# Kernel tuning notes

Measured on AMD Instinct MI355X. Metric: run time of the kernel, lower is better.

Reference implementation:

```python
import jax, jax.numpy as jnp
import numpy as np

NUM_GRAPHS = 2048


def gcn_conv(x, W, b, edge, N):
    # PyG GCNConv: x' = D^{-1/2} (A + I) D^{-1/2} (x W) + b
    src, dst = edge[0], edge[1]
    loop = jnp.arange(N, dtype=src.dtype)
    src = jnp.concatenate([src, loop])
    dst = jnp.concatenate([dst, loop])
    h = x @ W  # [N, out]
    deg = jax.ops.segment_sum(jnp.ones(dst.shape, x.dtype), dst, num_segments=N)
    dinv = jnp.where(deg > 0, jax.lax.rsqrt(deg), 0.0)
    norm = dinv[src] * dinv[dst]  # [E+N]
    out = jax.ops.segment_sum(h[src] * norm[:, None], dst, num_segments=N)
    return out + b


def pool_max_mean(x, batch, G):
    mx = jax.ops.segment_max(x, batch, num_segments=G)
    mx = jnp.where(jnp.isfinite(mx), mx, 0.0)  # guard empty segments
    s = jax.ops.segment_sum(x, batch, num_segments=G)
    cnt = jax.ops.segment_sum(jnp.ones((x.shape[0],), x.dtype), batch, num_segments=G)
    mean = s / jnp.maximum(cnt, 1.0)[:, None]
    return mx, mean


def setup_inputs() -> dict:
    key = jax.random.key(0)
    ks = jax.random.split(key, 20)
    F, CE, SE, DD = 64, 64, 32, 128
    Nc, Ec, Ns, Es = 100000, 1250000, 100000, 1250000

    def glorot(k, shape):
        fan_in, fan_out = shape[0], shape[1]
        lim = np.sqrt(6.0 / (fan_in + fan_out)).astype(np.float32)
        return jax.random.uniform(k, shape, jnp.float32, -lim, lim)

    inp = {
        "c": jax.random.normal(ks[0], (Nc, F), jnp.float32),
        "c_edge": jax.random.randint(ks[1], (2, Ec), 0, Nc),
        "c_batch": jnp.sort(jax.random.randint(ks[2], (Nc,), 0, NUM_GRAPHS)),
        "s": jax.random.normal(ks[3], (Ns, F), jnp.float32),
        "s_edge": jax.random.randint(ks[4], (2, Es), 0, Ns),
        "s_batch": jnp.sort(jax.random.randint(ks[5], (Ns,), 0, NUM_GRAPHS)),
        "Wc0": glorot(ks[6], (F, CE)), "bc0": jnp.zeros((CE,), jnp.float32),
        "Wc1": glorot(ks[7], (CE, CE)), "bc1": jnp.zeros((CE,), jnp.float32),
        "Wc2": glorot(ks[8], (CE, CE)), "bc2": jnp.zeros((CE,), jnp.float32),
        "Ws0": glorot(ks[9], (F, SE)), "bs0": jnp.zeros((SE,), jnp.float32),
        "Ws1": glorot(ks[10], (SE, SE)), "bs1": jnp.zeros((SE,), jnp.float32),
        "Ws2": glorot(ks[11], (SE, SE)), "bs2": jnp.zeros((SE,), jnp.float32),
        "Wd": glorot(ks[12], ((CE + SE) * 2, DD)), "bd": jnp.zeros((DD,), jnp.float32),
        "Wo": glorot(ks[13], (DD, 1)), "bo": jnp.zeros((1,), jnp.float32),
    }
    return inp


def reference(c, c_edge, c_batch, s, s_edge, s_batch,
              Wc0, bc0, Wc1, bc1, Wc2, bc2,
              Ws0, bs0, Ws1, bs1, Ws2, bs2,
              Wd, bd, Wo, bo):
    Nc, Ns = c.shape[0], s.shape[0]
    cro = jax.nn.relu(gcn_conv(c, Wc0, bc0, c_edge, Nc))
    cro = jax.nn.relu(gcn_conv(cro, Wc1, bc1, c_edge, Nc))
    cro = jax.nn.relu(gcn_conv(cro, Wc2, bc2, c_edge, Nc))
    solv = jax.nn.relu(gcn_conv(s, Ws0, bs0, s_edge, Ns))
    solv = jax.nn.relu(gcn_conv(solv, Ws1, bs1, s_edge, Ns))
    solv = jax.nn.relu(gcn_conv(solv, Ws2, bs2, s_edge, Ns))
    c_mx, c_mean = pool_max_mean(cro, c_batch, NUM_GRAPHS)
    s_mx, s_mean = pool_max_mean(solv, s_batch, NUM_GRAPHS)
    embed = jnp.concatenate([c_mx, c_mean, s_mx, s_mean], axis=1)  # [G, 192]
    dense = jax.nn.relu(embed @ Wd + bd)
    out = dense @ Wo + bo  # [G, 1]
    return out, embed
```

## Files before the change

kernel.cpp:

```cpp
#include <hip/hip_runtime.h>
#include <hip/hip_fp16.h>
#include <math.h>


static inline int cdiv(int a, int b) { return (a + b - 1) / b; }

#define BUCKET_CAP 8192
#define P1_CHUNK   4096

__global__ void zero_int(int* __restrict__ p, int n) {
    int i = blockIdx.x * blockDim.x + threadIdx.x;
    if (i < n) p[i] = 0;
}

__global__ __launch_bounds__(256) void p1_partition(const int* __restrict__ c_edge, int Ec,
                                                    const int* __restrict__ s_edge, int Es,
                                                    int Nc_pad, int Etot, int nbuck,
                                                    int* __restrict__ bucket_fill,
                                                    unsigned* __restrict__ pk) {
    __shared__ unsigned       wbuf[P1_CHUNK];
    __shared__ unsigned short bbuf[P1_CHUNK];
    __shared__ int            hist[512];
    int e0 = blockIdx.x * P1_CHUNK;
    int n  = Etot - e0;
    if (n > P1_CHUNK) n = P1_CHUNK;
    for (int i = threadIdx.x; i < nbuck; i += 256) hist[i] = 0;
    __syncthreads();
    for (int i = threadIdx.x; i < n; i += 256) {
        int e = e0 + i, src, g;
        if (e < Ec) { src = c_edge[e]; g = c_edge[Ec + e]; }
        else        { int e2 = e - Ec; src = s_edge[e2]; g = Nc_pad + s_edge[Es + e2]; }
        int b   = g >> 9;
        wbuf[i] = ((unsigned)(g & 511) << 17) | (unsigned)src;
        bbuf[i] = (unsigned short)b;
        atomicAdd(&hist[b], 1);
    }
    __syncthreads();
    for (int i = threadIdx.x; i < nbuck; i += 256) {
        int h = hist[i];
        hist[i] = h ? atomicAdd(&bucket_fill[i], h) : 0;
    }
    __syncthreads();
    for (int i = threadIdx.x; i < n; i += 256) {
        int b    = bbuf[i];
        int slot = atomicAdd(&hist[b], 1);
        if (slot < BUCKET_CAP) pk[(size_t)b * BUCKET_CAP + slot] = wbuf[i];
    }
}

__global__ __launch_bounds__(512) void p2_scanbuckets(const int* __restrict__ fill, int nbuck,
                                                      int* __restrict__ basearr,
                                                      int* __restrict__ off_all, int Ntot_pad, int Etot) {
    __shared__ int sh[512];
    int v = (threadIdx.x < nbuck) ? fill[threadIdx.x] : 0;
    sh[threadIdx.x] = v;
    __syncthreads();
    for (int ofs = 1; ofs < 512; ofs <<= 1) {
        int t = (threadIdx.x >= ofs) ? sh[threadIdx.x - ofs] : 0;
        __syncthreads();
        sh[threadIdx.x] += t;
        __syncthreads();
    }
    if (threadIdx.x < nbuck) basearr[threadIdx.x] = sh[threadIdx.x] - v;
    if (threadIdx.x == 0) off_all[Ntot_pad] = Etot;
}

__global__ __launch_bounds__(512) void p3_build(const unsigned* __restrict__ pk,
                                                const int* __restrict__ fillarr,
                                                const int* __restrict__ basearr,
                                                int* __restrict__ off_all,
                                                float* __restrict__ dinv,
                                                int* __restrict__ csr) {
    __shared__ int sh[512];
    int b    = blockIdx.x;
    int fill = fillarr[b];
    if (fill > BUCKET_CAP) fill = BUCKET_CAP;
    int base = basearr[b];
    const unsigned* reg = pk + (size_t)b * BUCKET_CAP;
    sh[threadIdx.x] = 0;
    __syncthreads();
    for (int i = threadIdx.x; i < fill; i += 512) atomicAdd(&sh[reg[i] >> 17], 1);
    __syncthreads();
    int cnt = sh[threadIdx.x];
    for (int ofs = 1; ofs < 512; ofs <<= 1) {
        int t = (threadIdx.x >= ofs) ? sh[threadIdx.x - ofs] : 0;
        __syncthreads();
        sh[threadIdx.x] += t;
        __syncthreads();
    }
    int excl = sh[threadIdx.x] - cnt;
    int node = b * 512 + threadIdx.x;
    off_all[node] = base + excl;
    dinv[node]    = rsqrtf((float)(cnt + 1));
    __syncthreads();
    sh[threadIdx.x] = excl;
    __syncthreads();
    for (int i = threadIdx.x; i < fill; i += 512) {
        unsigned w    = reg[i];
        int      slot = atomicAdd(&sh[w >> 17], 1);
        csr[base + slot] = (int)(w & 0x1FFFFu);
    }
}

template <int K, int M, typename TIN>
__device__ void gemm_body(int bid, const TIN* __restrict__ X, const float* __restrict__ W,
                          const float* __restrict__ dinv, __half* __restrict__ H, int N,
                          char* smem_) {
    constexpr int CG = M / 4, RG = 256 / CG, RB = RG * 4, RBP = RB + 4;
    float* Xs = (float*)smem_;
    float* Ws = Xs + K * RBP;
    const int t    = threadIdx.x;
    const int row0 = bid * RB;

    for (int idx = t; idx < K * M; idx += 256) Ws[idx] = W[idx];

    if constexpr (sizeof(TIN) == 4) {
        constexpr int NF4 = RB * K / 4;
        for (int idx = t; idx < NF4; idx += 256) {
            int row = idx / (K / 4), k4 = idx % (K / 4);
            float4 v = make_float4(0.f, 0.f, 0.f, 0.f);
            int gr = row0 + row;
            if (gr < N) v = *(const float4*)((const float*)X + (size_t)gr * K + k4 * 4);
            Xs[(k4 * 4 + 0) * RBP + row] = v.x;
            Xs[(k4 * 4 + 1) * RBP + row] = v.y;
            Xs[(k4 * 4 + 2) * RBP + row] = v.z;
            Xs[(k4 * 4 + 3) * RBP + row] = v.w;
        }
    } else {
        constexpr int NF8 = RB * K / 8;
        for (int idx = t; idx < NF8; idx += 256) {
            int row = idx / (K / 8), k8 = idx % (K / 8);
            int gr = row0 + row;
            union { float4 f4; __half2 h2[4]; } u;
            u.f4 = make_float4(0.f, 0.f, 0.f, 0.f);
            if (gr < N) u.f4 = *(const float4*)((const __half*)X + (size_t)gr * K + k8 * 8);
#pragma unroll
            for (int q = 0; q < 4; ++q) {
                float2 pq = __half22float2(u.h2[q]);
                Xs[(k8 * 8 + 2 * q + 0) * RBP + row] = pq.x;
                Xs[(k8 * 8 + 2 * q + 1) * RBP + row] = pq.y;
            }
        }
    }
    __syncthreads();

    const int cc = t % CG, rr = t / CG;
    float acc[4][4] = {};
#pragma unroll 4
    for (int k = 0; k < K; k++) {
        float4 xv = *(const float4*)(Xs + k * RBP + rr * 4);
        float4 wv = *(const float4*)(Ws + k * M + cc * 4);
        acc[0][0] += xv.x * wv.x; acc[0][1] += xv.x * wv.y; acc[0][2] += xv.x * wv.z; acc[0][3] += xv.x * wv.w;
        acc[1][0] += xv.y * wv.x; acc[1][1] += xv.y * wv.y; acc[1][2] += xv.y * wv.z; acc[1][3] += xv.y * wv.w;
        acc[2][0] += xv.z * wv.x; acc[2][1] += xv.z * wv.y; acc[2][2] += xv.z * wv.z; acc[2][3] += xv.z * wv.w;
        acc[3][0] += xv.w * wv.x; acc[3][1] += xv.w * wv.y; acc[3][2] += xv.w * wv.z; acc[3][3] += xv.w * wv.w;
    }

#pragma unroll
    for (int i = 0; i < 4; i++) {
        int gr = row0 + rr * 4 + i;
        if (gr < N) {
            float sc = dinv[gr];
            __half2* dp = (__half2*)(H + (size_t)gr * M + cc * 4);
            dp[0] = __floats2half2_rn(acc[i][0] * sc, acc[i][1] * sc);
            dp[1] = __floats2half2_rn(acc[i][2] * sc, acc[i][3] * sc);
        }
    }
}

__device__ __forceinline__ float4 load4h(const float2* __restrict__ base, size_t idx) {
    float2 r = base[idx];
    union { float2 f2; __half2 h2[2]; } u;
    u.f2 = r;
    float2 a = __half22float2(u.h2[0]);
    float2 b = __half22float2(u.h2[1]);
    return make_float4(a.x, a.y, b.x, b.y);
}

template <int M>
__device__ void agg_body(int bid, const __half* __restrict__ H,
                         const int* __restrict__ off_g,
                         const int* __restrict__ csr,
                         const float* __restrict__ dinv_g,
                         const float* __restrict__ b,
                         __half* __restrict__ out, int Nloc) {
    constexpr int L   = M / 4;
    constexpr int NPW = 64 / L;
    int lane = threadIdx.x & 63;
    int wave = threadIdx.x >> 6;
    int fq   = lane & (L - 1);
    int sub  = lane / L;
    int node = (bid * 4 + wave) * NPW + sub;
    if (node >= Nloc) return;
    const float2* H4 = (const float2*)H;
    int j0 = off_g[node], j1 = off_g[node + 1];
    float4 acc = load4h(H4, (size_t)node * L + fq);
    int j = j0;
    for (; j + 8 <= j1; j += 8) {
        int s0 = csr[j],     s1 = csr[j + 1], s2 = csr[j + 2], s3 = csr[j + 3];
        int s4 = csr[j + 4], s5 = csr[j + 5], s6 = csr[j + 6], s7 = csr[j + 7];
        float4 a0 = load4h(H4, (size_t)s0 * L + fq);
        float4 a1 = load4h(H4, (size_t)s1 * L + fq);
        float4 a2 = load4h(H4, (size_t)s2 * L + fq);
        float4 a3 = load4h(H4, (size_t)s3 * L + fq);
        float4 a4 = load4h(H4, (size_t)s4 * L + fq);
        float4 a5 = load4h(H4, (size_t)s5 * L + fq);
        float4 a6 = load4h(H4, (size_t)s6 * L + fq);
        float4 a7 = load4h(H4, (size_t)s7 * L + fq);
        acc.x += (a0.x + a1.x + a2.x + a3.x) + (a4.x + a5.x + a6.x + a7.x);
        acc.y += (a0.y + a1.y + a2.y + a3.y) + (a4.y + a5.y + a6.y + a7.y);
        acc.z += (a0.z + a1.z + a2.z + a3.z) + (a4.z + a5.z + a6.z + a7.z);
        acc.w += (a0.w + a1.w + a2.w + a3.w) + (a4.w + a5.w + a6.w + a7.w);
    }
    for (; j + 4 <= j1; j += 4) {
        int s0 = csr[j], s1 = csr[j + 1], s2 = csr[j + 2], s3 = csr[j + 3];
        float4 a0 = load4h(H4, (size_t)s0 * L + fq);
        float4 a1 = load4h(H4, (size_t)s1 * L + fq);
        float4 a2 = load4h(H4, (size_t)s2 * L + fq);
        float4 a3 = load4h(H4, (size_t)s3 * L + fq);
        acc.x += a0.x + a1.x + a2.x + a3.x;
        acc.y += a0.y + a1.y + a2.y + a3.y;
        acc.z += a0.z + a1.z + a2.z + a3.z;
        acc.w += a0.w + a1.w + a2.w + a3.w;
    }
    for (; j < j1; ++j) {
        float4 a = load4h(H4, (size_t)csr[j] * L + fq);
        acc.x += a.x; acc.y += a.y; acc.z += a.z; acc.w += a.w;
    }
    float  dv = dinv_g[node];
    float4 bb = ((const float4*)b)[fq];
    float  vx = dv * acc.x + bb.x;
    float  vy = dv * acc.y + bb.y;
    float  vz = dv * acc.z + bb.z;
    float  vw = dv * acc.w + bb.w;
    union { float2 f2; __half2 h2[2]; } o;
    o.h2[0] = __floats2half2_rn(vx > 0.f ? vx : 0.f, vy > 0.f ? vy : 0.f);
    o.h2[1] = __floats2half2_rn(vz > 0.f ? vz : 0.f, vw > 0.f ? vw : 0.f);
    ((float2*)out)[(size_t)node * L + fq] = o.f2;
}

__global__ __launch_bounds__(256) void gemmBoth0(const float* __restrict__ Xc, const float* __restrict__ Wc,
                                                 __half* __restrict__ cH, int Nc,
                                                 const float* __restrict__ Xs, const float* __restrict__ Ws,
                                                 __half* __restrict__ sH, int Ns,
                                                 const float* __restrict__ dinv_all, int Nc_pad, int nbC) {
    __shared__ __align__(16) char smem[41984];
    if (blockIdx.x < nbC) gemm_body<64, 64, float>(blockIdx.x, Xc, Wc, dinv_all, cH, Nc, smem);
    else                  gemm_body<64, 32, float>(blockIdx.x - nbC, Xs, Ws, dinv_all + Nc_pad, sH, Ns, smem);
}

__global__ __launch_bounds__(256) void gemmBoth(const __half* __restrict__ Xc, const float* __restrict__ Wc,
                                                __half* __restrict__ cH, int Nc,
                                                const __half* __restrict__ Xs, const float* __restrict__ Ws,
                                                __half* __restrict__ sH, int Ns,
                                                const float* __restrict__ dinv_all, int Nc_pad, int nbC) {
    __shared__ __align__(16) char smem[34816];
    if (blockIdx.x < nbC) gemm_body<64, 64, __half>(blockIdx.x, Xc, Wc, dinv_all, cH, Nc, smem);
    else                  gemm_body<32, 32, __half>(blockIdx.x - nbC, Xs, Ws, dinv_all + Nc_pad, sH, Ns, smem);
}

__global__ __launch_bounds__(256) void aggBoth(const __half* __restrict__ cH, const __half* __restrict__ sH,
                                               const int* __restrict__ off_all, const int* __restrict__ csr_all,
                                               const float* __restrict__ dinv_all,
                                               const float* __restrict__ bc, const float* __restrict__ bs,
                                               __half* __restrict__ outc, __half* __restrict__ outs,
                                               int Nc, int Ns, int Nc_pad, int nbC) {
    if (blockIdx.x < nbC)
        agg_body<64>(blockIdx.x, cH, off_all, csr_all, dinv_all, bc, outc, Nc);
    else
        agg_body<32>(blockIdx.x - nbC, sH, off_all + Nc_pad, csr_all,
                     dinv_all + Nc_pad, bs, outs, Ns);
}

__device__ __forceinline__ int lbound(const int* __restrict__ a, int n, int key) {
    int lo = 0, hi = n;
    while (lo < hi) {
        int mid = (lo + hi) >> 1;
        if (a[mid] < key) lo = mid + 1; else hi = mid;
    }
    return lo;
}

__global__ __launch_bounds__(128) void poolDense(const __half* __restrict__ cX, const int* __restrict__ c_batch, int Nc,
                                                 const __half* __restrict__ sX, const int* __restrict__ s_batch, int Ns,
                                                 const float* __restrict__ Wd, const float* __restrict__ bd,
                                                 const float* __restrict__ Wo, const float* __restrict__ bo,
                                                 float* __restrict__ outv, float* __restrict__ embed) {
    __shared__ float e[192];
    __shared__ float red[128];
    int g = blockIdx.x, t = threadIdx.x;
    if (t < 64) {
        int lo = lbound(c_batch, Nc, g), hi = lbound(c_batch, Nc, g + 1);
        float mx = 0.f, sm = 0.f;
        for (int i = lo; i < hi; ++i) {
            float v = __half2float(cX[(size_t)i * 64 + t]);
            mx = fmaxf(mx, v); sm += v;
        }
        int cn = hi - lo;
        e[t]      = mx;
        e[64 + t] = sm / (float)(cn > 0 ? cn : 1);
    } else if (t < 96) {
        int f  = t - 64;
        int lo = lbound(s_batch, Ns, g), hi = lbound(s_batch, Ns, g + 1);
        float mx = 0.f, sm = 0.f;
        for (int i = lo; i < hi; ++i) {
            float v = __half2float(sX[(size_t)i * 32 + f]);
            mx = fmaxf(mx, v); sm += v;
        }
        int cn = hi - lo;
        e[128 + f] = mx;
        e[160 + f] = sm / (float)(cn > 0 ? cn : 1);
    }
    __syncthreads();
    for (int k = t; k < 192; k += 128) embed[(size_t)g * 192 + k] = e[k];
    float acc = bd[t];
    for (int k = 0; k < 192; ++k) acc += e[k] * Wd[k * 128 + t];
    float d = acc > 0.f ? acc : 0.f;
    red[t]  = d * Wo[t];
    __syncthreads();
    for (int ofs = 64; ofs > 0; ofs >>= 1) {
        if (t < ofs) red[t] += red[t + ofs];
        __syncthreads();
    }
    if (t == 0) outv[g] = red[0] + bo[0];
}


extern "C" void kernel_launch(void* const* d_in, const int* in_sizes, int n_in,
                              void* d_out, int out_size, void* d_ws, size_t ws_size,
                              hipStream_t stream) {
    const float* c       = (const float*)d_in[0];
    const int*   c_edge  = (const int*)d_in[1];
    const int*   c_batch = (const int*)d_in[2];
    const float* s       = (const float*)d_in[3];
    const int*   s_edge  = (const int*)d_in[4];
    const int*   s_batch = (const int*)d_in[5];
    const float* Wc0 = (const float*)d_in[6],  *bc0 = (const float*)d_in[7];
    const float* Wc1 = (const float*)d_in[8],  *bc1 = (const float*)d_in[9];
    const float* Wc2 = (const float*)d_in[10], *bc2 = (const float*)d_in[11];
    const float* Ws0 = (const float*)d_in[12], *bs0 = (const float*)d_in[13];
    const float* Ws1 = (const float*)d_in[14], *bs1 = (const float*)d_in[15];
    const float* Ws2 = (const float*)d_in[16], *bs2 = (const float*)d_in[17];
    const float* Wd  = (const float*)d_in[18], *bd  = (const float*)d_in[19];
    const float* Wo  = (const float*)d_in[20], *bo  = (const float*)d_in[21];

    const int Nc = in_sizes[0] / 64;
    const int Ec = in_sizes[1] / 2;
    const int Ns = in_sizes[3] / 64;
    const int Es = in_sizes[4] / 2;
    const int G  = out_size / 193;
    const int Nc_pad   = cdiv(Nc, 512) * 512;
    const int Ns_pad   = cdiv(Ns, 512) * 512;
    const int Ntot_pad = Nc_pad + Ns_pad;
    const int Etot     = Ec + Es;
    const int nbuck    = Ntot_pad >> 9;

    char* p = (char*)d_ws;
    auto  alloc = [&](size_t bytes) -> void* {
        void* r = (void*)p;
        p += (bytes + 255) & ~(size_t)255;
        return r;
    };
    int*      bucket_fill = (int*)alloc(512 * 4);
    int*      bucket_base = (int*)alloc(512 * 4);
    unsigned* pk          = (unsigned*)alloc((size_t)nbuck * BUCKET_CAP * 4);
    int*      off_all     = (int*)alloc(((size_t)Ntot_pad + 1) * 4);
    int*      csr_all     = (int*)alloc((size_t)Etot * 4);
    float*    dinv_all    = (float*)alloc((size_t)Ntot_pad * 4);
    __half*   bufC        = (__half*)alloc((size_t)Nc * 64 * 2);
    __half*   bufS        = (__half*)alloc((size_t)Ns * 32 * 2);
    __half*   cH          = (__half*)alloc((size_t)Nc * 64 * 2);
    __half*   sH          = (__half*)alloc((size_t)Ns * 32 * 2);

    float* outv  = (float*)d_out;
    float* embed = outv + G;

    const int nbGmC = cdiv(Nc, 64), nbGm0S = cdiv(Ns, 128), nbGmS = cdiv(Ns, 128);
    const int nbAgC = Nc_pad / 16,  nbAgS  = Ns_pad / 32;

    zero_int<<<cdiv(nbuck, 256), 256, 0, stream>>>(bucket_fill, nbuck);
    p1_partition<<<cdiv(Etot, P1_CHUNK), 256, 0, stream>>>(c_edge, Ec, s_edge, Es,
                                                           Nc_pad, Etot, nbuck, bucket_fill, pk);
    p2_scanbuckets<<<1, 512, 0, stream>>>(bucket_fill, nbuck, bucket_base, off_all, Ntot_pad, Etot);
    p3_build<<<nbuck, 512, 0, stream>>>(pk, bucket_fill, bucket_base,
                                        off_all, dinv_all, csr_all);

    gemmBoth0<<<nbGmC + nbGm0S, 256, 0, stream>>>(c, Wc0, cH, Nc, s, Ws0, sH, Ns,
                                                  dinv_all, Nc_pad, nbGmC);
    aggBoth<<<nbAgC + nbAgS, 256, 0, stream>>>(cH, sH, off_all, csr_all, dinv_all,
                                               bc0, bs0, bufC, bufS, Nc, Ns, Nc_pad, nbAgC);
    gemmBoth<<<nbGmC + nbGmS, 256, 0, stream>>>(bufC, Wc1, cH, Nc, bufS, Ws1, sH, Ns,
                                                dinv_all, Nc_pad, nbGmC);
    aggBoth<<<nbAgC + nbAgS, 256, 0, stream>>>(cH, sH, off_all, csr_all, dinv_all,
                                               bc1, bs1, bufC, bufS, Nc, Ns, Nc_pad, nbAgC);
    gemmBoth<<<nbGmC + nbGmS, 256, 0, stream>>>(bufC, Wc2, cH, Nc, bufS, Ws2, sH, Ns,
                                                dinv_all, Nc_pad, nbGmC);
    aggBoth<<<nbAgC + nbAgS, 256, 0, stream>>>(cH, sH, off_all, csr_all, dinv_all,
                                               bc2, bs2, bufC, bufS, Nc, Ns, Nc_pad, nbAgC);

    poolDense<<<G, 128, 0, stream>>>(bufC, c_batch, Nc, bufS, s_batch, Ns,
                                     Wd, bd, Wo, bo, outv, embed);
}
```

Baseline: 418.2 us.

## Replace scalar FP32 GEMM with MFMA f16 matrix-core GEMM for GCN transforms

Rewrites the per-layer dense transform (X·W scaled by dinv) to use the 16x16x32 f16 MFMA instruction. X tiles are staged in LDS as half precision and W is pre-swizzled into the MFMA B-operand layout, replacing the 4x4 register-blocked FP32 FMA loop. This cuts ALU time and LDS footprint. In exchange, the first layer's FP32 inputs and the weights are rounded to fp16, and the output is written as scattered single-half stores, which coalesce less well.

Result: faster. 367.6 us (-12.1%).

```diff
diff --git a/kernel.cpp b/kernel.cpp
--- a/kernel.cpp
+++ b/kernel.cpp
@@ -7,6 +7,9 @@
 
 #define BUCKET_CAP 8192
 #define P1_CHUNK   4096
+
+typedef _Float16 v8h __attribute__((ext_vector_type(8)));
+typedef float    v4f __attribute__((ext_vector_type(4)));
 
 __global__ void zero_int(int* __restrict__ p, int n) {
     int i = blockIdx.x * blockDim.x + threadIdx.x;
@@ -103,67 +106,79 @@
 }
 
 template <int K, int M, typename TIN>
-__device__ void gemm_body(int bid, const TIN* __restrict__ X, const float* __restrict__ W,
+__device__ void gemm_mfma(int bid, const TIN* __restrict__ X, const float* __restrict__ W,
                           const float* __restrict__ dinv, __half* __restrict__ H, int N,
                           char* smem_) {
-    constexpr int CG = M / 4, RG = 256 / CG, RB = RG * 4, RBP = RB + 4;
-    float* Xs = (float*)smem_;
-    float* Ws = Xs + K * RBP;
+    constexpr int RB = 64;
+    constexpr int KP = K + 8;
+    constexpr int NT = M / 16;
+    constexpr int KS = K / 32;
+    _Float16* Xh = (_Float16*)smem_;
+    _Float16* Wz = Xh + RB * KP;
     const int t    = threadIdx.x;
     const int row0 = bid * RB;
 
-    for (int idx = t; idx < K * M; idx += 256) Ws[idx] = W[idx];
-
+    constexpr int WENT = NT * KS * 64;
+    for (int idx = t; idx < WENT; idx += 256) {
+        int lane = idx & 63, rest = idx >> 6;
+        int ks = rest % KS, ntl = rest / KS;
+        int kbase = ks * 32 + (lane >> 4) * 8;
+        int col   = ntl * 16 + (lane & 15);
+        union { float4 f4; _Float16 h[8]; } u;
+#pragma unroll
+        for (int j = 0; j < 8; ++j) u.h[j] = (_Float16)W[(kbase + j) * M + col];
+        *(float4*)(Wz + idx * 8) = u.f4;
+    }
     if constexpr (sizeof(TIN) == 4) {
-        constexpr int NF4 = RB * K / 4;
-        for (int idx = t; idx < NF4; idx += 256) {
+        constexpr int NI = RB * K / 4;
+        for (int idx = t; idx < NI; idx += 256) {
             int row = idx / (K / 4), k4 = idx % (K / 4);
+            int gr = row0 + row;
             float4 v = make_float4(0.f, 0.f, 0.f, 0.f);
-            int gr = row0 + row;
             if (gr < N) v = *(const float4*)((const float*)X + (size_t)gr * K + k4 * 4);
-            Xs[(k4 * 4 + 0) * RBP + row] = v.x;
-            Xs[(k4 * 4 + 1) * RBP + row] = v.y;
-            Xs[(k4 * 4 + 2) * RBP + row] = v.z;
-            Xs[(k4 * 4 + 3) * RBP + row] = v.w;
+            union { float2 f2; _Float16 h[4]; } u;
+            u.h[0] = (_Float16)v.x; u.h[1] = (_Float16)v.y;
+            u.h[2] = (_Float16)v.z; u.h[3] = (_Float16)v.w;
+            *(float2*)(Xh + row * KP + k4 * 4) = u.f2;
         }
     } else {
-        constexpr int NF8 = RB * K / 8;
-        for (int idx = t; idx < NF8; idx += 256) {
+        constexpr int NI = RB * K / 8;
+        for (int idx = t; idx < NI; idx += 256) {
             int row = idx / (K / 8), k8 = idx % (K / 8);
             int gr = row0 + row;
-            union { float4 f4; __half2 h2[4]; } u;
-            u.f4 = make_float4(0.f, 0.f, 0.f, 0.f);
-            if (gr < N) u.f4 = *(const float4*)((const __half*)X + (size_t)gr * K + k8 * 8);
-#pragma unroll
-            for (int q = 0; q < 4; ++q) {
-                float2 pq = __half22float2(u.h2[q]);
-                Xs[(k8 * 8 + 2 * q + 0) * RBP + row] = pq.x;
-                Xs[(k8 * 8 + 2 * q + 1) * RBP + row] = pq.y;
-            }
-        }
-    }
-    __syncthreads();
-
-    const int cc = t % CG, rr = t / CG;
-    float acc[4][4] = {};
-#pragma unroll 4
-    for (int k = 0; k < K; k++) {
-        float4 xv = *(const float4*)(Xs + k * RBP + rr * 4);
-        float4 wv = *(const float4*)(Ws + k * M + cc * 4);
-        acc[0][0] += xv.x * wv.x; acc[0][1] += xv.x * wv.y; acc[0][2] += xv.x * wv.z; acc[0][3] += xv.x * wv.w;
-        acc[1][0] += xv.y * wv.x; acc[1][1] += xv.y * wv.y; acc[1][2] += xv.y * wv.z; acc[1][3] += xv.y * wv.w;
-        acc[2][0] += xv.z * wv.x; acc[2][1] += xv.z * wv.y; acc[2][2] += xv.z * wv.z; acc[2][3] += xv.z * wv.w;
-        acc[3][0] += xv.w * wv.x; acc[3][1] += xv.w * wv.y; acc[3][2] += xv.w * wv.z; acc[3][3] += xv.w * wv.w;
-    }
-
-#pragma unroll
-    for (int i = 0; i < 4; i++) {
-        int gr = row0 + rr * 4 + i;
+            float4 v = make_float4(0.f, 0.f, 0.f, 0.f);
+            if (gr < N) v = *(const float4*)((const __half*)X + (size_t)gr * K + k8 * 8);
+            *(float4*)(Xh + row * KP + k8 * 8) = v;
+        }
+    }
+    __syncthreads();
+
+    const int wave = t >> 6, lane = t & 63;
+    const int quad = lane >> 4, nl = lane & 15;
+    const int rowA = wave * 16 + nl;
+
+    v4f acc[NT];
+#pragma unroll
+    for (int i = 0; i < NT; ++i) acc[i] = (v4f){0.f, 0.f, 0.f, 0.f};
+
+#pragma unroll
+    for (int ks = 0; ks < KS; ++ks) {
+        v8h a = *(const v8h*)(Xh + rowA * KP + ks * 32 + quad * 8);
+#pragma unroll
+        for (int ntl = 0; ntl < NT; ++ntl) {
+            v8h b = *(const v8h*)(Wz + ((ntl * KS + ks) * 64 + lane) * 8);
+            acc[ntl] = __builtin_amdgcn_mfma_f32_16x16x32_f16(a, b, acc[ntl], 0, 0, 0);
+        }
+    }
+
+#pragma unroll
+    for (int r = 0; r < 4; ++r) {
+        int gr = row0 + wave * 16 + quad * 4 + r;
         if (gr < N) {
-            float sc = dinv[gr];
-            __half2* dp = (__half2*)(H + (size_t)gr * M + cc * 4);
-            dp[0] = __floats2half2_rn(acc[i][0] * sc, acc[i][1] * sc);
-            dp[1] = __floats2half2_rn(acc[i][2] * sc, acc[i][3] * sc);
+            float dv = dinv[gr];
+#pragma unroll
+            for (int ntl = 0; ntl < NT; ++ntl)
+                H[(size_t)gr * M + ntl * 16 + nl] = __float2half(acc[ntl][r] * dv);
         }
     }
 }
@@ -244,9 +259,9 @@
                                                  const float* __restrict__ Xs, const float* __restrict__ Ws,
                                                  __half* __restrict__ sH, int Ns,
                                                  const float* __restrict__ dinv_all, int Nc_pad, int nbC) {
-    __shared__ __align__(16) char smem[41984];
-    if (blockIdx.x < nbC) gemm_body<64, 64, float>(blockIdx.x, Xc, Wc, dinv_all, cH, Nc, smem);
-    else                  gemm_body<64, 32, float>(blockIdx.x - nbC, Xs, Ws, dinv_all + Nc_pad, sH, Ns, smem);
+    __shared__ __align__(16) char smem[17408];
+    if (blockIdx.x < nbC) gemm_mfma<64, 64, float>(blockIdx.x, Xc, Wc, dinv_all, cH, Nc, smem);
+    else                  gemm_mfma<64, 32, float>(blockIdx.x - nbC, Xs, Ws, dinv_all + Nc_pad, sH, Ns, smem);
 }
 
 __global__ __launch_bounds__(256) void gemmBoth(const __half* __restrict__ Xc, const float* __restrict__ Wc,
@@ -254,9 +269,9 @@
                                                 const __half* __restrict__ Xs, const float* __restrict__ Ws,
                                                 __half* __restrict__ sH, int Ns,
                                                 const float* __restrict__ dinv_all, int Nc_pad, int nbC) {
-    __shared__ __align__(16) char smem[34816];
-    if (blockIdx.x < nbC) gemm_body<64, 64, __half>(blockIdx.x, Xc, Wc, dinv_all, cH, Nc, smem);
-    else                  gemm_body<32, 32, __half>(blockIdx.x - nbC, Xs, Ws, dinv_all + Nc_pad, sH, Ns, smem);
+    __shared__ __align__(16) char smem[17408];
+    if (blockIdx.x < nbC) gemm_mfma<64, 64, __half>(blockIdx.x, Xc, Wc, dinv_all, cH, Nc, smem);
+    else                  gemm_mfma<32, 32, __half>(blockIdx.x - nbC, Xs, Ws, dinv_all + Nc_pad, sH, Ns, smem);
 }
 
 __global__ __launch_bounds__(256) void aggBoth(const __half* __restrict__ cH, const __half* __restrict__ sH,
@@ -375,8 +390,8 @@
     float* outv  = (float*)d_out;
     float* embed = outv + G;
 
-    const int nbGmC = cdiv(Nc, 64), nbGm0S = cdiv(Ns, 128), nbGmS = cdiv(Ns, 128);
-    const int nbAgC = Nc_pad / 16,  nbAgS  = Ns_pad / 32;
+    const int nbGmC = cdiv(Nc, 64), nbGmS = cdiv(Ns, 64);
+    const int nbAgC = Nc_pad / 16,  nbAgS = Ns_pad / 32;
 
     zero_int<<<cdiv(nbuck, 256), 256, 0, stream>>>(bucket_fill, nbuck);
     p1_partition<<<cdiv(Etot, P1_CHUNK), 256, 0, stream>>>(c_edge, Ec, s_edge, Es,
@@ -385,8 +400,8 @@
     p3_build<<<nbuck, 512, 0, stream>>>(pk, bucket_fill, bucket_base,
                                         off_all, dinv_all, csr_all);
 
-    gemmBoth0<<<nbGmC + nbGm0S, 256, 0, stream>>>(c, Wc0, cH, Nc, s, Ws0, sH, Ns,
-                                                  dinv_all, Nc_pad, nbGmC);
+    gemmBoth0<<<nbGmC + nbGmS, 256, 0, stream>>>(c, Wc0, cH, Nc, s, Ws0, sH, Ns,
+                                                 dinv_all, Nc_pad, nbGmC);
     aggBoth<<<nbAgC + nbAgS, 256, 0, stream>>>(cH, sH, off_all, csr_all, dinv_all,
                                                bc0, bs0, bufC, bufS, Nc, Ns, Nc_pad, nbAgC);
     gemmBoth<<<nbGmC + nbGmS, 256, 0, stream>>>(bufC, Wc1, cH, Nc, bufS, Ws1, sH, Ns,
```
